# Kernel tuning notes

Hardware: AMD Instinct MI355X
Metric: run time of the kernel (lower is better)

## Reference

```python
import jax, jax.numpy as jnp
import numpy as np

K = 40        # knn neighbors (hard-coded in forward)
BN_EPS = 1e-5
NEG_SLOPE = 0.2
NHEADS = 8
ADIM = 64
HDIM = NHEADS * ADIM  # 512
SCALE = HDIM ** (-0.5)  # note: original scales by hdim**-0.5, not adim**-0.5


def knn_idx(x, k):
    # x: (B, C, N) -> (B, N, k) indices of k nearest neighbors (incl. self)
    xx = jnp.sum(x * x, axis=1)                       # (B, N)
    inner = jnp.einsum('bcn,bcm->bnm', x, x)          # (B, N, N)
    neg_sq_dist = 2.0 * inner - xx[:, :, None] - xx[:, None, :]
    return jax.lax.top_k(neg_sq_dist, k)[1]           # (B, N, k)


def get_graph_feature(x, k):
    # x: (B, C, N) -> (B, 2C, N, k)
    idx = knn_idx(x, k)                               # (B, N, k) int32
    xt = jnp.transpose(x, (0, 2, 1))                  # (B, N, C)
    feat = jax.vmap(lambda pts, ids: pts[ids])(xt, idx)  # (B, N, k, C)
    center = xt[:, :, None, :]                        # (B, N, 1, C)
    out = jnp.concatenate(
        [feat - center, jnp.broadcast_to(center, feat.shape)], axis=-1)
    return jnp.transpose(out, (0, 3, 1, 2))           # (B, 2C, N, k)


def bn_lrelu(h, g, b, m, v):
    # inference-mode BatchNorm2d over channel axis=1 + LeakyReLU(0.2)
    scale = g / jnp.sqrt(v + BN_EPS)
    h = (h - m[None, :, None, None]) * scale[None, :, None, None] + b[None, :, None, None]
    return jax.nn.leaky_relu(h, NEG_SLOPE)


def branch(p, conv5_w, bn5_g, bn5_b, bn5_m, bn5_v, conv6_w, bn6_g, bn6_b, bn6_m, bn6_v):
    g = get_graph_feature(p, K)                       # (B, 1024, N, k)
    h = jnp.einsum('oc,bcnk->bonk', conv5_w, g)       # (B, 512, N, k)
    h = bn_lrelu(h, bn5_g, bn5_b, bn5_m, bn5_v)
    h = jnp.transpose(h, (0, 2, 1, 3))                # (B, N=2048, 512, k)
    h = jnp.einsum('oc,bcnk->bonk', conv6_w, h)       # (B, 515, 512, k)
    h = bn_lrelu(h, bn6_g, bn6_b, bn6_m, bn6_v)
    h = jnp.transpose(h, (0, 2, 1, 3))                # (B, 512, 515, k)
    return jnp.max(h, axis=-1)                        # (B, 512, 515)


def heads(f, W):
    # f: (B, S, indim), W: (hdim, indim) -> (B, nheads, S, adim)
    q = jnp.einsum('bsi,oi->bso', f, W)
    B, S, _ = q.shape
    return jnp.transpose(q.reshape(B, S, NHEADS, ADIM), (0, 2, 1, 3))


def setup_inputs() -> dict:
    key = jax.random.key(0)
    ks = jax.random.split(key, 8)
    B, C, N = 1, 512, 2048
    indim = 515
    inp = {
        'x': jax.random.normal(ks[0], (B, C, N), jnp.float32),
        'y': jax.random.normal(ks[1], (B, C, N), jnp.float32),
        'conv5_w': jax.random.normal(ks[2], (512, 1024), jnp.float32) * 0.02,
        'bn5_g': jnp.ones((512,), jnp.float32),
        'bn5_b': jnp.zeros((512,), jnp.float32),
        'bn5_m': jnp.zeros((512,), jnp.float32),
        'bn5_v': jnp.ones((512,), jnp.float32),
        'conv6_w': jax.random.normal(ks[3], (515, 2048), jnp.float32) * 0.02,
        'bn6_g': jnp.ones((515,), jnp.float32),
        'bn6_b': jnp.zeros((515,), jnp.float32),
        'bn6_m': jnp.zeros((515,), jnp.float32),
        'bn6_v': jnp.ones((515,), jnp.float32),
        'Wq': jax.random.normal(ks[4], (HDIM, indim), jnp.float32) * 0.02,
        'Wk': jax.random.normal(ks[5], (HDIM, indim), jnp.float32) * 0.02,
        'Wv': jax.random.normal(ks[6], (HDIM, indim), jnp.float32) * 0.02,
        'Wout': jax.random.normal(ks[7], (indim, HDIM), jnp.float32) * 0.02,
        'bout': jnp.zeros((indim,), jnp.float32),
    }
    return inp


def reference(x, y, conv5_w, bn5_g, bn5_b, bn5_m, bn5_v,
              conv6_w, bn6_g, bn6_b, bn6_m, bn6_v,
              Wq, Wk, Wv, Wout, bout):
    xf = branch(x, conv5_w, bn5_g, bn5_b, bn5_m, bn5_v,
                conv6_w, bn6_g, bn6_b, bn6_m, bn6_v)   # (B, 512, 515)
    yf = branch(y, conv5_w, bn5_g, bn5_b, bn5_m, bn5_v,
                conv6_w, bn6_g, bn6_b, bn6_m, bn6_v)   # (B, 512, 515)
    q = heads(xf, Wq)                                  # (B, H, 512, adim)
    k = heads(yf, Wk)
    v = heads(yf, Wv)
    scores = jax.nn.softmax(jnp.einsum('bhsd,bhtd->bhst', q, k) * SCALE, axis=-1)
    weighted = jnp.einsum('bhst,bhtd->bhsd', scores, v)  # (B, H, 512, adim)
    B, H, S, D = weighted.shape
    merged = jnp.transpose(weighted, (0, 2, 1, 3)).reshape(B, S, H * D)
    return jnp.einsum('bsh,oh->bso', merged, Wout) + bout  # (B, 512, 515)
```

## Files before the change

### kernel.cpp

```cpp
#include <hip/hip_runtime.h>
#include <hip/hip_bf16.h>

typedef __bf16 bf16_t;
typedef float f32x4 __attribute__((ext_vector_type(4)));
typedef __bf16 bf16x8 __attribute__((ext_vector_type(8)));

#define ASYNC_COPY16(gptr, lptr) \
    __builtin_amdgcn_global_load_lds((const __attribute__((address_space(1))) void*)(gptr), \
                                     (__attribute__((address_space(3))) void*)(lptr), 16, 0, 0)

__device__ __forceinline__ float ldx(const void* p, long i, int isbf) {
    return isbf ? (float)((const bf16_t*)p)[i] : ((const float*)p)[i];
}

__global__ __launch_bounds__(256)
void detect_dtype(const void* __restrict__ x, int n, int* __restrict__ flags)
{
    __shared__ int red[4];
    const int tid = threadIdx.x;
    const int ns = n < 8192 ? n : 8192;
    int cnt = 0;
    for (int i = tid; i < ns; i += 256) {
        float v = (float)((const bf16_t*)x)[i];
        float a = fabsf(v);
        bool pl = (v == 0.f) || (a >= 6e-8f && a <= 1.7e7f);
        cnt += pl ? 1 : 0;
    }
    for (int o = 32; o; o >>= 1) cnt += __shfl_down(cnt, o);
    if ((tid & 63) == 0) red[tid >> 6] = cnt;
    __syncthreads();
    if (tid == 0) {
        int t = red[0] + red[1] + red[2] + red[3];
        flags[0] = (t * 10 >= ns * 9) ? 1 : 0;
    }
}

__global__ __launch_bounds__(256)
void conv_elem(const void* __restrict__ src, bf16_t* __restrict__ dst, int n,
               const int* __restrict__ flag)
{
    const int isbf = *flag;
    for (long i = blockIdx.x * 256L + threadIdx.x; i < n; i += (long)gridDim.x * 256)
        dst[i] = (bf16_t)ldx(src, i, isbf);
}

struct P9 { const void* p[9]; int n[9]; };
__global__ __launch_bounds__(256)
void conv_param(P9 pk, float* __restrict__ dst, const int* __restrict__ flag)
{
    const int isbf = *flag;
    const int b = blockIdx.x, n = pk.n[b];
    for (int j = threadIdx.x; j < n; j += 256)
        dst[b * 544 + j] = ldx(pk.p[b], j, isbf);
}

__global__ __launch_bounds__(256)
void pad_wf(const void* __restrict__ W, bf16_t* __restrict__ Wp, const int* __restrict__ flag)
{
    const int isbf = *flag;
    const long i = blockIdx.x * 256L + threadIdx.x;
    if (i >= 512 * 544) return;
    const long o = i / 544, c = i % 544;
    Wp[i] = (c < 515) ? (bf16_t)ldx(W, o * 515 + c, isbf) : (bf16_t)0.f;
}

__global__ __launch_bounds__(256)
void transpose_split(const void* __restrict__ X, bf16_t* __restrict__ XtA,
                     bf16_t* __restrict__ XtB, const int* __restrict__ flag)
{
    __shared__ __align__(16) bf16_t thi[32][33];
    __shared__ __align__(16) bf16_t tlo[32][33];
    const int isbf = *flag;
    const int n0 = blockIdx.x * 32, c0 = blockIdx.y * 32;
    const int lx = threadIdx.x & 31, ly = threadIdx.x >> 5;
    for (int i = 0; i < 4; ++i) {
        float v = ldx(X, (long)(c0 + ly + i * 8) * 2048 + n0 + lx, isbf);
        bf16_t hi = (bf16_t)v;
        thi[ly + i * 8][lx] = hi;
        tlo[ly + i * 8][lx] = (bf16_t)(v - (float)hi);
    }
    __syncthreads();
    for (int i = 0; i < 4; ++i) {
        const long n = n0 + ly + i * 8;
        const int c = c0 + lx;
        bf16_t hi = thi[lx][ly + i * 8], lo = tlo[lx][ly + i * 8];
        XtA[n * 1536 + c] = hi;  XtA[n * 1536 + 512 + c] = lo;  XtA[n * 1536 + 1024 + c] = hi;
        XtB[n * 1536 + c] = hi;  XtB[n * 1536 + 512 + c] = hi;  XtB[n * 1536 + 1024 + c] = lo;
    }
}

__global__ __launch_bounds__(256)
void xx_kernel(const bf16_t* __restrict__ XtA, float* __restrict__ xx)
{
    const long n = blockIdx.x * 256L + threadIdx.x;
    float acc = 0.f;
    for (int c = 0; c < 512; ++c) {
        float v = (float)XtA[n * 1536 + c] + (float)XtA[n * 1536 + 512 + c];
        acc += v * v;
    }
    xx[n] = acc;
}

__global__ __launch_bounds__(256)
void gemm128d(const bf16_t* __restrict__ A, const bf16_t* __restrict__ B,
              float* __restrict__ C, int M, int N, int K, int lda, int ldb, int ldc)
{
    __shared__ __align__(16) bf16_t As[2][4096];
    __shared__ __align__(16) bf16_t Bs[2][4096];
    const int tid = threadIdx.x;
    const int m0 = blockIdx.x * 128, n0 = blockIdx.y * 128;
    const int wave = tid >> 6, lane = tid & 63;
    const int wm = (wave >> 1) * 64, wn = (wave & 1) * 64;
    const int l15 = lane & 15, quad = lane >> 4;

    const bf16_t* ga[2]; const bf16_t* gb[2]; int loff[2];
    for (int i = 0; i < 2; ++i) {
        const int q = wave * 2 + i;
        const int seg = q & 3, half = q >> 2;
        const int row = half * 64 + lane;
        long ar = min((long)(m0 + row), (long)M - 1);
        long br = min((long)(n0 + row), (long)N - 1);
        ga[i] = A + ar * lda + seg * 8;
        gb[i] = B + br * ldb + seg * 8;
        loff[i] = seg * 1024 + half * 512;
    }

    f32x4 acc[4][4] = {};

    for (int i = 0; i < 2; ++i) {
        ASYNC_COPY16(ga[i], &As[0][loff[i]]);
        ASYNC_COPY16(gb[i], &Bs[0][loff[i]]);
    }

    for (int k0 = 0; k0 < K; k0 += 32) {
        const int cur = (k0 >> 5) & 1;
        __syncthreads();
        if (k0 + 32 < K) {
            for (int i = 0; i < 2; ++i) {
                ASYNC_COPY16(ga[i] + k0 + 32, &As[cur ^ 1][loff[i]]);
                ASYNC_COPY16(gb[i] + k0 + 32, &Bs[cur ^ 1][loff[i]]);
            }
        }
        bf16x8 af[4], bfr[4];
        for (int mi = 0; mi < 4; ++mi)
            af[mi] = *(const bf16x8*)&As[cur][quad * 1024 + (wm + mi * 16 + l15) * 8];
        for (int ni = 0; ni < 4; ++ni)
            bfr[ni] = *(const bf16x8*)&Bs[cur][quad * 1024 + (wn + ni * 16 + l15) * 8];
        for (int mi = 0; mi < 4; ++mi)
        for (int ni = 0; ni < 4; ++ni)
            acc[mi][ni] = __builtin_amdgcn_mfma_f32_16x16x32_bf16(af[mi], bfr[ni], acc[mi][ni], 0, 0, 0);
    }

    for (int mi = 0; mi < 4; ++mi)
    for (int ni = 0; ni < 4; ++ni)
    for (int r = 0; r < 4; ++r) {
        int gm = m0 + wm + mi * 16 + quad * 4 + r;
        int gn = n0 + wn + ni * 16 + l15;
        if (gm >= M || gn >= N) continue;
        C[(long)gm * ldc + gn] = acc[mi][ni][r];
    }
}

__global__ __launch_bounds__(256)
void gemm64d(const bf16_t* __restrict__ A, const bf16_t* __restrict__ B,
             float* __restrict__ C, const float* __restrict__ xx,
             int M, int N, int K, int lda, int ldb, int ldc,
             long aBS, long bBS, long cBS, int epi, int moff)
{
    __shared__ __align__(16) bf16_t As[2][4 * 64 * 8];
    __shared__ __align__(16) bf16_t Bs[2][4 * 64 * 8];
    const int tid = threadIdx.x;
    const int m0 = blockIdx.y * 64, n0 = blockIdx.x * 64;
    const int bz = blockIdx.z;
    A += (long)bz * aBS;
    B += (long)bz * bBS;
    const int wave = tid >> 6, lane = tid & 63;
    const int wm = (wave >> 1) * 32, wn = (wave & 1) * 32;
    const int l15 = lane & 15, quad = lane >> 4;

    const long ar = min((long)(m0 + lane), (long)M - 1);
    const long br = min((long)(n0 + lane), (long)N - 1);
    const bf16_t* ga = A + ar * lda + wave * 8;
    const bf16_t* gb = B + br * ldb + wave * 8;

    f32x4 acc[2][2] = {};

    ASYNC_COPY16(ga, &As[0][wave * 512]);
    ASYNC_COPY16(gb, &Bs[0][wave * 512]);

    for (int k0 = 0; k0 < K; k0 += 32) {
        const int cur = (k0 >> 5) & 1;
        __syncthreads();
        if (k0 + 32 < K) {
            ASYNC_COPY16(ga + k0 + 32, &As[cur ^ 1][wave * 512]);
            ASYNC_COPY16(gb + k0 + 32, &Bs[cur ^ 1][wave * 512]);
        }
        bf16x8 af0 = *(const bf16x8*)&As[cur][quad * 512 + (wm +      l15) * 8];
        bf16x8 af1 = *(const bf16x8*)&As[cur][quad * 512 + (wm + 16 + l15) * 8];
        bf16x8 bf0 = *(const bf16x8*)&Bs[cur][quad * 512 + (wn +      l15) * 8];
        bf16x8 bf1 = *(const bf16x8*)&Bs[cur][quad * 512 + (wn + 16 + l15) * 8];
        acc[0][0] = __builtin_amdgcn_mfma_f32_16x16x32_bf16(af0, bf0, acc[0][0], 0, 0, 0);
        acc[0][1] = __builtin_amdgcn_mfma_f32_16x16x32_bf16(af0, bf1, acc[0][1], 0, 0, 0);
        acc[1][0] = __builtin_amdgcn_mfma_f32_16x16x32_bf16(af1, bf0, acc[1][0], 0, 0, 0);
        acc[1][1] = __builtin_amdgcn_mfma_f32_16x16x32_bf16(af1, bf1, acc[1][1], 0, 0, 0);
    }

    C += (long)bz * cBS;
    for (int mi = 0; mi < 2; ++mi)
    for (int ni = 0; ni < 2; ++ni)
    for (int r = 0; r < 4; ++r) {
        int gm = m0 + wm + mi * 16 + quad * 4 + r;
        int gn = n0 + wn + ni * 16 + l15;
        if (gm >= M || gn >= N) continue;
        float o = acc[mi][ni][r];
        long cidx = (long)gm * ldc + gn;
        if (epi == 1) C[cidx] = 2.f * o - xx[gm + moff] - xx[gn];
        else          C[cidx] = o;
    }
}

__global__ __launch_bounds__(256)
void gemm_nt(const bf16_t* __restrict__ A, const bf16_t* __restrict__ B,
             void* __restrict__ Cv, const float* __restrict__ bias,
             const int* __restrict__ oflag, float alpha,
             int M, int N, int K, int lda, int ldb, int ldc,
             long aBS, long bBS, long cBS, int epi)
{
    __shared__ __align__(16) bf16_t As[64 * 40];
    __shared__ __align__(16) bf16_t Bs[64 * 40];
    const int tid = threadIdx.x;
    const int m0 = blockIdx.y * 64, n0 = blockIdx.x * 64;
    const int bz = blockIdx.z;
    A += (long)bz * aBS;
    B += (long)bz * bBS;

    const int lrow = tid >> 2;
    const int lseg = (tid & 3) * 8;
    const long arow = min(m0 + lrow, M - 1);
    const long brow = min(n0 + lrow, N - 1);
    const bf16_t* ap = A + arow * lda + lseg;
    const bf16_t* bp = B + brow * ldb + lseg;

    const int wave = tid >> 6, lane = tid & 63;
    const int wm = (wave >> 1) * 32, wn = (wave & 1) * 32;
    const int l15 = lane & 15, quad = lane >> 4;

    f32x4 acc[2][2] = {};

    for (int k0 = 0; k0 < K; k0 += 32) {
        int4 av = *(const int4*)ap;  ap += 32;
        int4 bv = *(const int4*)bp;  bp += 32;
        __syncthreads();
        *(int4*)(&As[lrow * 40 + lseg]) = av;
        *(int4*)(&Bs[lrow * 40 + lseg]) = bv;
        __syncthreads();
        bf16x8 af0 = *(const bf16x8*)(&As[(wm +      l15) * 40 + quad * 8]);
        bf16x8 af1 = *(const bf16x8*)(&As[(wm + 16 + l15) * 40 + quad * 8]);
        bf16x8 bf0 = *(const bf16x8*)(&Bs[(wn +      l15) * 40 + quad * 8]);
        bf16x8 bf1 = *(const bf16x8*)(&Bs[(wn + 16 + l15) * 40 + quad * 8]);
        acc[0][0] = __builtin_amdgcn_mfma_f32_16x16x32_bf16(af0, bf0, acc[0][0], 0, 0, 0);
        acc[0][1] = __builtin_amdgcn_mfma_f32_16x16x32_bf16(af0, bf1, acc[0][1], 0, 0, 0);
        acc[1][0] = __builtin_amdgcn_mfma_f32_16x16x32_bf16(af1, bf0, acc[1][0], 0, 0, 0);
        acc[1][1] = __builtin_amdgcn_mfma_f32_16x16x32_bf16(af1, bf1, acc[1][1], 0, 0, 0);
    }

    const int ofl = oflag ? *oflag : 1;
    for (int mi = 0; mi < 2; ++mi)
    for (int ni = 0; ni < 2; ++ni)
    for (int r = 0; r < 4; ++r) {
        int gm = m0 + wm + mi * 16 + quad * 4 + r;
        int gn = n0 + wn + ni * 16 + l15;
        if (gm >= M || gn >= N) continue;
        float o = acc[mi][ni][r];
        long cidx = (long)bz * cBS + (long)gm * ldc + gn;
        switch (epi) {
        case 2: ((bf16_t*)Cv)[cidx] = (bf16_t)o; break;
        case 3: ((float*)Cv)[cidx] = o * alpha; break;
        case 5: ((bf16_t*)Cv)[(long)bz * cBS + (long)gn * ldc + gm] = (bf16_t)o; break;
        case 6: {
            float w = o + bias[gn];
            if (ofl) ((bf16_t*)Cv)[cidx] = (bf16_t)w;
            else     ((float*)Cv)[cidx]  = w;
        } break;
        }
    }
}

__global__ __launch_bounds__(256)
void topk40_bs(const float* __restrict__ S, int* __restrict__ idx_out)
{
    __shared__ int red[4];
    __shared__ unsigned long long tmask[8][4];
    __shared__ int sh_slot;
    __shared__ unsigned cu[48];
    __shared__ int      ci[48];
    const int row = blockIdx.x, tid = threadIdx.x;
    const int wave = tid >> 6, lane = tid & 63;

    unsigned uvr[8];
    for (int c = 0; c < 8; ++c) {
        unsigned x = __float_as_uint(S[(long)row * 2048 + c * 256 + tid]);
        uvr[c] = (x & 0x80000000u) ? ~x : (x | 0x80000000u);
    }
    if (tid == 0) sh_slot = 0;

    unsigned lo = 0u, hi = 0xFFFFFFFFu;
    while (hi - lo > 1u) {
        unsigned mid = lo + ((hi - lo) >> 1);
        int c = 0;
        for (int i = 0; i < 8; ++i) c += (uvr[i] > mid) ? 1 : 0;
        for (int o = 32; o; o >>= 1) c += __shfl_down(c, o);
        if (lane == 0) red[wave] = c;
        __syncthreads();
        int tot = red[0] + red[1] + red[2] + red[3];
        __syncthreads();
        if (tot >= 40) lo = mid; else hi = mid;
    }
    const unsigned thr = hi;

    for (int c = 0; c < 8; ++c)
        if (uvr[c] > thr) {
            int s = atomicAdd(&sh_slot, 1);
            cu[s] = uvr[c]; ci[s] = c * 256 + tid;
        }
    for (int c = 0; c < 8; ++c) {
        unsigned long long m = __ballot(uvr[c] == thr);
        if (lane == 0) tmask[c][wave] = m;
    }
    __syncthreads();
    const int want = 40 - sh_slot;
    int base = 0;
    for (int c = 0; c < 8; ++c) {
        if (uvr[c] == thr) {
            int r = base;
            for (int w = 0; w < wave; ++w) r += __popcll(tmask[c][w]);
            r += __popcll(tmask[c][wave] & (((unsigned long long)1 << lane) - 1));
            if (r < want) {
                int s = atomicAdd(&sh_slot, 1);
                cu[s] = uvr[c]; ci[s] = c * 256 + tid;
            }
        }
        for (int w = 0; w < 4; ++w) base += __popcll(tmask[c][w]);
    }
    __syncthreads();
    if (tid < 40) {
        unsigned u = cu[tid]; int i = ci[tid];
        int r = 0;
        for (int j = 0; j < 40; ++j)
            r += (cu[j] > u || (cu[j] == u && ci[j] < i)) ? 1 : 0;
        idx_out[row * 40 + r] = i;
    }
}

__global__ __launch_bounds__(256)
void h1a_gen(const float* __restrict__ T, const float* __restrict__ U,
             const int* __restrict__ idx, const float* __restrict__ pf,
             bf16_t* __restrict__ Hc, int c0)
{
    __shared__ int idxs[40 * 256];
    const int c5 = c0 + blockIdx.y, n0 = blockIdx.x * 256, tid = threadIdx.x;
    for (int i = tid; i < 40 * 256; i += 256)
        idxs[(i % 40) * 256 + (i / 40)] = idx[n0 * 40 + i] & 2047;
    const float sc = pf[c5] / sqrtf(pf[3 * 544 + c5] + 1e-5f);
    const float mu = pf[2 * 544 + c5], bb = pf[1 * 544 + c5];
    const float q  = U[(long)c5 * 2048 + n0 + tid] - T[(long)c5 * 2048 + n0 + tid];
    const float* Trow = T + (long)c5 * 2048;
    __syncthreads();
    for (int k = 0; k < 40; ++k) {
        float h = Trow[idxs[k * 256 + tid]] + q;
        h = (h - mu) * sc + bb;
        h = h >= 0.f ? h : 0.2f * h;
        Hc[(long)(blockIdx.y * 40 + k) * 2048 + n0 + tid] = (bf16_t)h;
    }
}

__global__ __launch_bounds__(256)
void epi6_max(const float* __restrict__ C2c, const float* __restrict__ p6,
              bf16_t* __restrict__ Fb, int c0, int Nc)
{
    const int cl = blockIdx.x, tid = threadIdx.x;
    for (int o2 = tid; o2 < 544; o2 += 256) {
        float r = 0.f;
        if (o2 < 515) {
            const float sc = p6[o2] / sqrtf(p6[3 * 544 + o2] + 1e-5f);
            const float mu = p6[2 * 544 + o2], bb = p6[1 * 544 + o2];
            const float* p = C2c + (long)o2 * Nc + cl * 40;
            float mx = -__builtin_inff();
            for (int k = 0; k < 40; ++k) {
                float h = (p[k] - mu) * sc + bb;
                h = h >= 0.f ? h : 0.2f * h;
                mx = fmaxf(mx, h);
            }
            r = mx;
        }
        Fb[(long)(c0 + cl) * 544 + o2] = (bf16_t)r;
    }
}

__global__ __launch_bounds__(256)
void softmax_row(const float* __restrict__ Sc, bf16_t* __restrict__ P)
{
    __shared__ float red[4];
    const long r = blockIdx.x;
    const int tid = threadIdx.x, lane = tid & 63, wave = tid >> 6;
    const float* row = Sc + r * 512;
    float v0 = row[tid], v1 = row[tid + 256];
    float mx = fmaxf(v0, v1);
    for (int off = 32; off; off >>= 1) mx = fmaxf(mx, __shfl_down(mx, off));
    if (lane == 0) red[wave] = mx;
    __syncthreads();
    mx = fmaxf(fmaxf(red[0], red[1]), fmaxf(red[2], red[3]));
    __syncthreads();
    float e0 = expf(v0 - mx), e1 = expf(v1 - mx);
    float sm = e0 + e1;
    for (int off = 32; off; off >>= 1) sm += __shfl_down(sm, off);
    if (lane == 0) red[wave] = sm;
    __syncthreads();
    sm = red[0] + red[1] + red[2] + red[3];
    float inv = 1.f / sm;
    P[r * 512 + tid] = (bf16_t)(e0 * inv);
    P[r * 512 + tid + 256] = (bf16_t)(e1 * inv);
}

extern "C" void kernel_launch(void* const* d_in, const int* in_sizes, int n_in,
                              void* d_out, int out_size, void* d_ws, size_t ws_size,
                              hipStream_t stream)
{
    (void)in_sizes; (void)n_in; (void)out_size;

    char* wsb = (char*)d_ws;
    size_t pos = 0;
    auto alloc = [&](size_t bytes) -> char* {
        char* p = wsb + pos;
        pos += (bytes + 255) & ~(size_t)255;
        return p;
    };
    int*    flags = (int*)  alloc(256);
    int*    idx   = (int*)  alloc(2048 * 40 * 4);
    float*  xx    = (float*)alloc(2048 * 4);
    float*  T     = (float*)alloc((size_t)512 * 2048 * 4);
    float*  U     = (float*)alloc((size_t)512 * 2048 * 4);
    bf16_t* XtA   = (bf16_t*)alloc((size_t)2048 * 1536 * 2);
    bf16_t* XtB   = (bf16_t*)alloc((size_t)2048 * 1536 * 2);
    bf16_t* W5c   = (bf16_t*)alloc((size_t)512 * 1024 * 2);
    bf16_t* W6c   = (bf16_t*)alloc((size_t)515 * 2048 * 2);
    bf16_t* Woutc = (bf16_t*)alloc((size_t)515 * 512 * 2);
    bf16_t* Wqp   = (bf16_t*)alloc((size_t)512 * 544 * 2);
    bf16_t* Wkp   = (bf16_t*)alloc((size_t)512 * 544 * 2);
    bf16_t* Wvp   = (bf16_t*)alloc((size_t)512 * 544 * 2);
    float*  pf    = (float*)alloc((size_t)9 * 544 * 4);
    bf16_t* Fb[2];
    Fb[0] = (bf16_t*)alloc((size_t)512 * 544 * 2);
    Fb[1] = (bf16_t*)alloc((size_t)512 * 544 * 2);
    bf16_t* qb = (bf16_t*)alloc((size_t)512 * 512 * 2);
    bf16_t* kb = (bf16_t*)alloc((size_t)512 * 512 * 2);
    bf16_t* vt = (bf16_t*)alloc((size_t)512 * 512 * 2);
    bf16_t* mg = (bf16_t*)alloc((size_t)512 * 512 * 2);
    char* BIG = wsb + pos;
    size_t big = (ws_size > pos) ? (ws_size - pos) : 0;
    if (big < 3939840) return;

    const int CC = (big >= 126074880) ? 512 : (big >= 63037440) ? 256
                 : (big >= 31518720)  ? 128 : (big >= 15759360) ? 64
                 : (big >= 7879680)   ? 32  : 16;
    const int RC = (big >= 16777216) ? 2048 : (big >= 4194304) ? 512 : 128;
    const int AH = (big >= 12582912) ? 8 : 1;
    const int Nc = CC * 40;

    float*  S   = (float*)BIG;
    bf16_t* Hc  = (bf16_t*)BIG;
    float*  C2c = (float*)(BIG + (size_t)Nc * 2048 * 2);
    float*  scA = (float*)BIG;
    bf16_t* prA = (bf16_t*)(BIG + (size_t)AH * 512 * 512 * 4);

    detect_dtype<<<1, 256, 0, stream>>>(d_in[0], in_sizes[0], flags);
    conv_elem<<<1024, 256, 0, stream>>>(d_in[2], W5c, 512 * 1024, flags);
    conv_elem<<<1024, 256, 0, stream>>>(d_in[7], W6c, 515 * 2048, flags);
    conv_elem<<<1024, 256, 0, stream>>>(d_in[15], Woutc, 515 * 512, flags);
    pad_wf<<<1088, 256, 0, stream>>>(d_in[12], Wqp, flags);
    pad_wf<<<1088, 256, 0, stream>>>(d_in[13], Wkp, flags);
    pad_wf<<<1088, 256, 0, stream>>>(d_in[14], Wvp, flags);
    P9 pk;
    const int pidx[9] = {3, 4, 5, 6, 8, 9, 10, 11, 16};
    for (int i = 0; i < 9; ++i) { pk.p[i] = d_in[pidx[i]]; pk.n[i] = in_sizes[pidx[i]]; }
    conv_param<<<9, 256, 0, stream>>>(pk, pf, flags);

    for (int b = 0; b < 2; ++b) {
        transpose_split<<<dim3(64, 16), 256, 0, stream>>>(d_in[b], XtA, XtB, flags);
        xx_kernel<<<8, 256, 0, stream>>>(XtA, xx);
        for (int r0 = 0; r0 < 2048; r0 += RC) {
            gemm64d<<<dim3(32, RC / 64), 256, 0, stream>>>(XtA + (size_t)r0 * 1536, XtB, S,
                xx, RC, 2048, 1536, 1536, 1536, 2048, 0, 0, 0, 1, r0);
            topk40_bs<<<RC, 256, 0, stream>>>(S, idx + (size_t)r0 * 40);
        }
        gemm64d<<<dim3(32, 8, 2), 256, 0, stream>>>(W5c, XtA, T, nullptr,
            512, 2048, 512, 1024, 1536, 2048, 512, 0, (long)512 * 2048, 0, 0);
        for (int c0 = 0; c0 < 512; c0 += CC) {
            h1a_gen<<<dim3(8, CC), 256, 0, stream>>>(T, U, idx, pf, Hc, c0);
            gemm128d<<<dim3(5, Nc / 128), 256, 0, stream>>>(W6c, Hc, C2c,
                515, Nc, 2048, 2048, 2048, Nc);
            epi6_max<<<CC, 256, 0, stream>>>(C2c, pf + 4 * 544, Fb[b], c0, Nc);
        }
    }

    gemm_nt<<<dim3(8, 8, 1), 256, 0, stream>>>(Fb[0], Wqp, qb, nullptr, nullptr, 0.f,
        512, 512, 544, 544, 544, 512, 0, 0, 0, 2);
    gemm_nt<<<dim3(8, 8, 1), 256, 0, stream>>>(Fb[1], Wkp, kb, nullptr, nullptr, 0.f,
        512, 512, 544, 544, 544, 512, 0, 0, 0, 2);
    gemm_nt<<<dim3(8, 8, 1), 256, 0, stream>>>(Fb[1], Wvp, vt, nullptr, nullptr, 0.f,
        512, 512, 544, 544, 544, 512, 0, 0, 0, 5);

    const float SCALE = 0.04419417382415922f;
    if (AH == 8) {
        gemm_nt<<<dim3(8, 8, 8), 256, 0, stream>>>(qb, kb, scA, nullptr, nullptr, SCALE,
            512, 512, 64, 512, 512, 512, 64, 64, 262144, 3);
        softmax_row<<<4096, 256, 0, stream>>>(scA, prA);
        gemm_nt<<<dim3(1, 8, 8), 256, 0, stream>>>(prA, vt, mg, nullptr, nullptr, 0.f,
            512, 64, 512, 512, 512, 512, 262144, 32768, 64, 2);
    } else {
        for (int h = 0; h < 8; ++h) {
            gemm_nt<<<dim3(8, 8, 1), 256, 0, stream>>>(qb + h * 64, kb + h * 64, scA,
                nullptr, nullptr, SCALE, 512, 512, 64, 512, 512, 512, 0, 0, 0, 3);
            softmax_row<<<512, 256, 0, stream>>>(scA, prA);
            gemm_nt<<<dim3(1, 8, 1), 256, 0, stream>>>(prA, vt + (size_t)h * 64 * 512,
                mg + h * 64, nullptr, nullptr, 0.f,
                512, 64, 512, 512, 512, 512, 0, 0, 0, 2);
        }
    }
    gemm_nt<<<dim3(9, 8, 1), 256, 0, stream>>>(mg, Woutc, d_out, pf + 8 * 544, flags,
        0.f, 512, 515, 512, 512, 512, 515, 0, 0, 0, 6);
}
```

Baseline: 970.5 us.

## Fuse BN6+LeakyReLU+max-over-k into conv6 GEMM epilogue via atomicMax

The conv6 GEMM now applies batch-norm and LeakyReLU in its epilogue and reduces over the k neighbours with an order-preserving unsigned atomicMax into a per-batch buffer. This removes the fp32 C2c intermediate and the separate epi6_max pass, which cuts global memory traffic and frees workspace so larger chunk sizes fit. The tile mapping is also remapped so consecutive n-tiles spread across the XCDs. The cost is many atomic operations, plus extra init and conversion kernels.

```diff
diff --git a/kernel.cpp b/kernel.cpp
--- a/kernel.cpp
+++ b/kernel.cpp
@@ -102,13 +102,21 @@
 }
 
 __global__ __launch_bounds__(256)
-void gemm128d(const bf16_t* __restrict__ A, const bf16_t* __restrict__ B,
-              float* __restrict__ C, int M, int N, int K, int lda, int ldb, int ldc)
+void gemm128f(const bf16_t* __restrict__ A, const bf16_t* __restrict__ B,
+              unsigned* __restrict__ FbU, const float* __restrict__ p6,
+              int M, int N, int K, int lda, int ldb, int c0)
 {
     __shared__ __align__(16) bf16_t As[2][4096];
     __shared__ __align__(16) bf16_t Bs[2][4096];
     const int tid = threadIdx.x;
-    const int m0 = blockIdx.x * 128, n0 = blockIdx.y * 128;
+    int mt, nt;
+    if ((gridDim.y & 7) == 0) {
+        const int bid = blockIdx.y * gridDim.x + blockIdx.x;
+        const int xcd = bid & 7, s = bid >> 3;
+        mt = s % gridDim.x;
+        nt = xcd + 8 * (s / gridDim.x);
+    } else { mt = blockIdx.x; nt = blockIdx.y; }
+    const int m0 = mt * 128, n0 = nt * 128;
     const int wave = tid >> 6, lane = tid & 63;
     const int wm = (wave >> 1) * 64, wn = (wave & 1) * 64;
     const int l15 = lane & 15, quad = lane >> 4;
@@ -152,13 +160,43 @@
     }
 
     for (int mi = 0; mi < 4; ++mi)
-    for (int ni = 0; ni < 4; ++ni)
     for (int r = 0; r < 4; ++r) {
-        int gm = m0 + wm + mi * 16 + quad * 4 + r;
-        int gn = n0 + wn + ni * 16 + l15;
-        if (gm >= M || gn >= N) continue;
-        C[(long)gm * ldc + gn] = acc[mi][ni][r];
-    }
+        const int gm = m0 + wm + mi * 16 + quad * 4 + r;
+        if (gm >= M) continue;
+        const float sc = p6[gm] / sqrtf(p6[3 * 544 + gm] + 1e-5f);
+        const float mu = p6[2 * 544 + gm], bb = p6[1 * 544 + gm];
+        for (int ni = 0; ni < 4; ++ni) {
+            const int gn = n0 + wn + ni * 16 + l15;
+            if (gn >= N) continue;
+            float h = (acc[mi][ni][r] - mu) * sc + bb;
+            h = h >= 0.f ? h : 0.2f * h;
+            unsigned x = __float_as_uint(h);
+            unsigned su = (x & 0x80000000u) ? ~x : (x | 0x80000000u);
+            atomicMax(&FbU[(long)(c0 + gn / 40) * 544 + gm], su);
+        }
+    }
+}
+
+__global__ __launch_bounds__(256)
+void fbu_init(unsigned* __restrict__ FbU)
+{
+    const long i = blockIdx.x * 256L + threadIdx.x;
+    if (i < 512 * 544) FbU[i] = 0u;
+}
+
+__global__ __launch_bounds__(256)
+void fbu_to_bf16(const unsigned* __restrict__ FbU, bf16_t* __restrict__ Fb)
+{
+    const long i = blockIdx.x * 256L + threadIdx.x;
+    if (i >= 512 * 544) return;
+    const int o2 = (int)(i % 544);
+    float v = 0.f;
+    if (o2 < 515) {
+        unsigned u = FbU[i];
+        unsigned x = (u & 0x80000000u) ? (u ^ 0x80000000u) : ~u;
+        v = __uint_as_float(x);
+    }
+    Fb[i] = (bf16_t)v;
 }
 
 __global__ __launch_bounds__(256)
@@ -375,29 +413,6 @@
 }
 
 __global__ __launch_bounds__(256)
-void epi6_max(const float* __restrict__ C2c, const float* __restrict__ p6,
-              bf16_t* __restrict__ Fb, int c0, int Nc)
-{
-    const int cl = blockIdx.x, tid = threadIdx.x;
-    for (int o2 = tid; o2 < 544; o2 += 256) {
-        float r = 0.f;
-        if (o2 < 515) {
-            const float sc = p6[o2] / sqrtf(p6[3 * 544 + o2] + 1e-5f);
-            const float mu = p6[2 * 544 + o2], bb = p6[1 * 544 + o2];
-            const float* p = C2c + (long)o2 * Nc + cl * 40;
-            float mx = -__builtin_inff();
-            for (int k = 0; k < 40; ++k) {
-                float h = (p[k] - mu) * sc + bb;
-                h = h >= 0.f ? h : 0.2f * h;
-                mx = fmaxf(mx, h);
-            }
-            r = mx;
-        }
-        Fb[(long)(c0 + cl) * 544 + o2] = (bf16_t)r;
-    }
-}
-
-__global__ __launch_bounds__(256)
 void softmax_row(const float* __restrict__ Sc, bf16_t* __restrict__ P)
 {
     __shared__ float red[4];
@@ -426,7 +441,7 @@
                               void* d_out, int out_size, void* d_ws, size_t ws_size,
                               hipStream_t stream)
 {
-    (void)in_sizes; (void)n_in; (void)out_size;
+    (void)n_in; (void)out_size;
 
     char* wsb = (char*)d_ws;
     size_t pos = 0;
@@ -435,20 +450,21 @@
         pos += (bytes + 255) & ~(size_t)255;
         return p;
     };
-    int*    flags = (int*)  alloc(256);
-    int*    idx   = (int*)  alloc(2048 * 40 * 4);
-    float*  xx    = (float*)alloc(2048 * 4);
-    float*  T     = (float*)alloc((size_t)512 * 2048 * 4);
-    float*  U     = (float*)alloc((size_t)512 * 2048 * 4);
-    bf16_t* XtA   = (bf16_t*)alloc((size_t)2048 * 1536 * 2);
-    bf16_t* XtB   = (bf16_t*)alloc((size_t)2048 * 1536 * 2);
-    bf16_t* W5c   = (bf16_t*)alloc((size_t)512 * 1024 * 2);
-    bf16_t* W6c   = (bf16_t*)alloc((size_t)515 * 2048 * 2);
-    bf16_t* Woutc = (bf16_t*)alloc((size_t)515 * 512 * 2);
-    bf16_t* Wqp   = (bf16_t*)alloc((size_t)512 * 544 * 2);
-    bf16_t* Wkp   = (bf16_t*)alloc((size_t)512 * 544 * 2);
-    bf16_t* Wvp   = (bf16_t*)alloc((size_t)512 * 544 * 2);
-    float*  pf    = (float*)alloc((size_t)9 * 544 * 4);
+    int*      flags = (int*)     alloc(256);
+    int*      idx   = (int*)     alloc(2048 * 40 * 4);
+    float*    xx    = (float*)   alloc(2048 * 4);
+    float*    T     = (float*)   alloc((size_t)512 * 2048 * 4);
+    float*    U     = (float*)   alloc((size_t)512 * 2048 * 4);
+    bf16_t*   XtA   = (bf16_t*)  alloc((size_t)2048 * 1536 * 2);
+    bf16_t*   XtB   = (bf16_t*)  alloc((size_t)2048 * 1536 * 2);
+    bf16_t*   W5c   = (bf16_t*)  alloc((size_t)512 * 1024 * 2);
+    bf16_t*   W6c   = (bf16_t*)  alloc((size_t)515 * 2048 * 2);
+    bf16_t*   Woutc = (bf16_t*)  alloc((size_t)515 * 512 * 2);
+    bf16_t*   Wqp   = (bf16_t*)  alloc((size_t)512 * 544 * 2);
+    bf16_t*   Wkp   = (bf16_t*)  alloc((size_t)512 * 544 * 2);
+    bf16_t*   Wvp   = (bf16_t*)  alloc((size_t)512 * 544 * 2);
+    float*    pf    = (float*)   alloc((size_t)9 * 544 * 4);
+    unsigned* FbU   = (unsigned*)alloc((size_t)512 * 544 * 4);
     bf16_t* Fb[2];
     Fb[0] = (bf16_t*)alloc((size_t)512 * 544 * 2);
     Fb[1] = (bf16_t*)alloc((size_t)512 * 544 * 2);
@@ -460,16 +476,15 @@
     size_t big = (ws_size > pos) ? (ws_size - pos) : 0;
     if (big < 3939840) return;
 
-    const int CC = (big >= 126074880) ? 512 : (big >= 63037440) ? 256
-                 : (big >= 31518720)  ? 128 : (big >= 15759360) ? 64
-                 : (big >= 7879680)   ? 32  : 16;
+    const int CC = (big >= 83886080) ? 512 : (big >= 41943040) ? 256
+                 : (big >= 20971520) ? 128 : (big >= 10485760) ? 64
+                 : (big >= 5242880)  ? 32  : 16;
     const int RC = (big >= 16777216) ? 2048 : (big >= 4194304) ? 512 : 128;
     const int AH = (big >= 12582912) ? 8 : 1;
     const int Nc = CC * 40;
 
     float*  S   = (float*)BIG;
     bf16_t* Hc  = (bf16_t*)BIG;
-    float*  C2c = (float*)(BIG + (size_t)Nc * 2048 * 2);
     float*  scA = (float*)BIG;
     bf16_t* prA = (bf16_t*)(BIG + (size_t)AH * 512 * 512 * 4);
 
@@ -495,12 +510,13 @@
         }
         gemm64d<<<dim3(32, 8, 2), 256, 0, stream>>>(W5c, XtA, T, nullptr,
             512, 2048, 512, 1024, 1536, 2048, 512, 0, (long)512 * 2048, 0, 0);
+        fbu_init<<<1088, 256, 0, stream>>>(FbU);
         for (int c0 = 0; c0 < 512; c0 += CC) {
             h1a_gen<<<dim3(8, CC), 256, 0, stream>>>(T, U, idx, pf, Hc, c0);
-            gemm128d<<<dim3(5, Nc / 128), 256, 0, stream>>>(W6c, Hc, C2c,
-                515, Nc, 2048, 2048, 2048, Nc);
-            epi6_max<<<CC, 256, 0, stream>>>(C2c, pf + 4 * 544, Fb[b], c0, Nc);
-        }
+            gemm128f<<<dim3(5, Nc / 128), 256, 0, stream>>>(W6c, Hc, FbU, pf + 4 * 544,
+                515, Nc, 2048, 2048, 2048, c0);
+        }
+        fbu_to_bf16<<<1088, 256, 0, stream>>>(FbU, Fb[b]);
     }
 
     gemm_nt<<<dim3(8, 8, 1), 256, 0, stream>>>(Fb[0], Wqp, qb, nullptr, nullptr, 0.f,
```

Result: slower. 1.792 ms (+84.6%).
